# Performance work log

Hardware: AMD Instinct MI355X
Metric: run time of the kernel (lower is better)

Reference implementation:

```python
import jax, jax.numpy as jnp
import numpy as np

EMBED = 1024
NUM_EXPERTS = 8
ACTIVE = 2
HIDDEN = 4 * EMBED


def setup_inputs() -> dict:
    key = jax.random.key(0)
    ks = jax.random.split(key, 7)
    B, T = 4, 1024
    s1 = 1.0 / np.sqrt(EMBED)
    s2 = 1.0 / np.sqrt(HIDDEN)
    return {
        "x": jax.random.normal(ks[0], (B, T, EMBED), dtype=jnp.float32),
        # stacked expert weights, layout [in, out] (torch Linear applies x @ W.T + b)
        "W1": jax.random.uniform(ks[1], (NUM_EXPERTS, EMBED, HIDDEN), jnp.float32, -s1, s1),
        "b1": jax.random.uniform(ks[2], (NUM_EXPERTS, HIDDEN), jnp.float32, -s1, s1),
        "W2": jax.random.uniform(ks[3], (NUM_EXPERTS, HIDDEN, EMBED), jnp.float32, -s2, s2),
        "b2": jax.random.uniform(ks[4], (NUM_EXPERTS, EMBED), jnp.float32, -s2, s2),
        "Wr": jax.random.uniform(ks[5], (EMBED, NUM_EXPERTS), jnp.float32, -s1, s1),
        "br": jax.random.uniform(ks[6], (NUM_EXPERTS,), jnp.float32, -s1, s1),
    }


def reference(x, W1, b1, W2, b2, Wr, br):
    # ---- router (TopkRouter) ----
    scores = x @ Wr + br                                  # [B,T,E]
    topk_scores, indices = jax.lax.top_k(scores, ACTIVE)  # [B,T,K]
    # mask = zeros scattered with topk scores at topk positions (others stay 0),
    # then softmax over ALL experts (faithful to the reference's quirky softmax).
    one_hot = jax.nn.one_hot(indices, NUM_EXPERTS, dtype=scores.dtype)  # [B,T,K,E]
    mask = jnp.einsum('btke,btk->bte', one_hot, topk_scores)            # [B,T,E]
    router_output = jax.nn.softmax(mask, axis=-1)                       # [B,T,E]

    # ---- dense all-experts FFN (Expert): relu(x@W1+b1)@W2+b2 per expert ----
    h = jax.nn.relu(jnp.einsum('btd,edh->bteh', x, W1) + b1)            # [B,T,E,H]
    expert_outputs = jnp.einsum('bteh,ehd->bted', h, W2) + b2           # [B,T,E,D]

    # ---- weighted combine ----
    return jnp.einsum('bte,bted->btd', router_output, expert_outputs)   # [B,T,D]
```

## Files before the change

kernel.cpp:

```cpp
#include <hip/hip_runtime.h>
#include <hip/hip_bf16.h>
#include <cstdint>
#include <cstddef>

#define EMBED  1024
#define NEXP   8
#define HIDDEN 4096
#define TOKENS 4096

typedef __attribute__((ext_vector_type(8))) short bf16x8;
typedef __attribute__((ext_vector_type(4))) float f32x4;
using bf16 = __hip_bfloat16;

__device__ __forceinline__ void gload_lds16(const void* g, void* l) {
    __builtin_amdgcn_global_load_lds((const __attribute__((address_space(1))) void*)g,
                                     (__attribute__((address_space(3))) void*)l,
                                     16, 0, 0);
}

__device__ __forceinline__ int swz(int b) { return b ^ (((b >> 7) & 7) << 4); }

__global__ void cvt_kernel(const float* __restrict__ in, bf16* __restrict__ out, size_t n) {
    size_t i = ((size_t)blockIdx.x * blockDim.x + threadIdx.x) * 4;
    if (i + 3 < n) {
        float4 v = *(const float4*)(in + i);
        out[i + 0] = __float2bfloat16(v.x);
        out[i + 1] = __float2bfloat16(v.y);
        out[i + 2] = __float2bfloat16(v.z);
        out[i + 3] = __float2bfloat16(v.w);
    }
}

__global__ void transpose_cvt(const float* __restrict__ in, bf16* __restrict__ out,
                              int K, int N, size_t in_estride, size_t out_eoff, int ldo) {
    const int e = blockIdx.z;
    const float* ine = in + (size_t)e * in_estride;
    bf16* oute = out + (size_t)e * out_eoff;
    __shared__ float tile[32][33];
    const int n0 = blockIdx.x * 32, k0 = blockIdx.y * 32;
    const int tx = threadIdx.x, ty = threadIdx.y;
    #pragma unroll
    for (int i = ty; i < 32; i += 8)
        tile[i][tx] = ine[(size_t)(k0 + i) * N + n0 + tx];
    __syncthreads();
    #pragma unroll
    for (int i = ty; i < 32; i += 8)
        oute[(size_t)(n0 + i) * ldo + k0 + tx] = __float2bfloat16(tile[tx][i]);
}

__global__ void router_kernel(const float* __restrict__ x, const float* __restrict__ Wr,
                              const float* __restrict__ br, float* __restrict__ w) {
    const int t = blockIdx.x;
    const int lane = threadIdx.x;
    const float* xt = x + (size_t)t * EMBED;
    float s[NEXP];
    #pragma unroll
    for (int e = 0; e < NEXP; e++) s[e] = 0.f;
    for (int k = lane; k < EMBED; k += 64) {
        const float xv = xt[k];
        const float* wrk = Wr + (size_t)k * NEXP;
        #pragma unroll
        for (int e = 0; e < NEXP; e++) s[e] = fmaf(xv, wrk[e], s[e]);
    }
    #pragma unroll
    for (int e = 0; e < NEXP; e++) {
        #pragma unroll
        for (int off = 32; off >= 1; off >>= 1)
            s[e] += __shfl_xor(s[e], off);
    }
    if (lane == 0) {
        float sc[NEXP];
        #pragma unroll
        for (int e = 0; e < NEXP; e++) sc[e] = s[e] + br[e];
        int i1 = 0; float m1 = sc[0];
        #pragma unroll
        for (int e = 1; e < NEXP; e++) if (sc[e] > m1) { m1 = sc[e]; i1 = e; }
        int i2 = -1; float m2 = -1e30f;
        #pragma unroll
        for (int e = 0; e < NEXP; e++) if (e != i1 && sc[e] > m2) { m2 = sc[e]; i2 = e; }
        const float mx = fmaxf(m1, 0.f);
        const float denom = 6.f * expf(0.f - mx) + expf(m1 - mx) + expf(m2 - mx);
        #pragma unroll
        for (int e = 0; e < NEXP; e++) {
            float v = (e == i1) ? m1 : ((e == i2) ? m2 : 0.f);
            w[(size_t)t * NEXP + e] = expf(v - mx) / denom;
        }
    }
}


#define BARX()  { __builtin_amdgcn_sched_barrier(0); __builtin_amdgcn_s_barrier(); __builtin_amdgcn_sched_barrier(0); }
#define LGKM0() { asm volatile("s_waitcnt lgkmcnt(0)" ::: "memory"); __builtin_amdgcn_sched_barrier(0); }

#define PIPE_PREAMBLE(Abase, Bbase, lda, ldb)                                        \
    __shared__ __align__(16) bf16 As[2][2][128 * 64];                                \
    __shared__ __align__(16) bf16 Bs[2][2][128 * 64];                                \
    const int tid = threadIdx.x;                                                     \
    const int lane = tid & 63, wid = tid >> 6;                                       \
    const int mhalf = wid >> 2, wB = wid & 3;                                        \
    const int nhalf = wB >> 1, nsub = wB & 1;                                        \
    const int wv_r = mhalf * 128, wv_c = wB * 64;                                    \
    f32x4 acc[8][4] = {};                                                            \
    int rowloc[2], colel[2];                                                         \
    _Pragma("unroll")                                                                \
    for (int j = 0; j < 2; j++) {                                                    \
        int bs = swz(tid * 16 + j * 8192);                                           \
        rowloc[j] = bs >> 7; colel[j] = (bs & 127) >> 1;                             \
    }                                                                                \
    const bf16* pA0 = (Abase) + (size_t)(brow + rowloc[0]) * (lda) + colel[0];       \
    const bf16* pA1 = (Abase) + (size_t)(brow + rowloc[1]) * (lda) + colel[1];       \
    const bf16* pB0 = (Bbase) + (size_t)(bcol + rowloc[0]) * (ldb) + colel[0];       \
    const bf16* pB1 = (Bbase) + (size_t)(bcol + rowloc[1]) * (ldb) + colel[1];       \
    const int fr = lane & 15, kb0 = (lane >> 4) * 16;                                \
    const int xm = (fr & 7) << 4;                                                    \
    const int baA0 = (fr * 128 + kb0) ^ xm, baA1 = (fr * 128 + kb0 + 64) ^ xm;       \
    const int brB = (nsub * 64 + fr) * 128;                                          \
    const int baB0 = (brB + kb0) ^ xm, baB1 = (brB + kb0 + 64) ^ xm;

#define STAGE_A(bi, h, koff, lda)                                                    \
    do {                                                                             \
        gload_lds16(pA0 + (size_t)(h) * 128 * (lda) + (koff), &As[bi][h][tid * 8]);  \
        gload_lds16(pA1 + (size_t)(h) * 128 * (lda) + (koff), &As[bi][h][tid * 8 + 4096]); \
    } while (0)
#define STAGE_B(bi, h, koff, ldb)                                                    \
    do {                                                                             \
        gload_lds16(pB0 + (size_t)(h) * 128 * (ldb) + (koff), &Bs[bi][h][tid * 8]);  \
        gload_lds16(pB1 + (size_t)(h) * 128 * (ldb) + (koff), &Bs[bi][h][tid * 8 + 4096]); \
    } while (0)

#define MFMA_Q(mh, nh)                                                               \
    __builtin_amdgcn_s_setprio(1);                                                   \
    _Pragma("unroll")                                                                \
    for (int mm = 0; mm < 4; mm++)                                                   \
        _Pragma("unroll")                                                            \
        for (int nn = 0; nn < 2; nn++) {                                             \
            acc[(mh)*4+mm][(nh)*2+nn] = __builtin_amdgcn_mfma_f32_16x16x32_bf16(     \
                a[(mh)*4+mm][0], b[(nh)*2+nn][0], acc[(mh)*4+mm][(nh)*2+nn], 0,0,0); \
            acc[(mh)*4+mm][(nh)*2+nn] = __builtin_amdgcn_mfma_f32_16x16x32_bf16(     \
                a[(mh)*4+mm][1], b[(nh)*2+nn][1], acc[(mh)*4+mm][(nh)*2+nn], 0,0,0); \
        }                                                                            \
    __builtin_amdgcn_s_setprio(0);

#define PIPE_KLOOP(NT, lda, ldb)                                                     \
    STAGE_A(0, 0, 0, lda); STAGE_A(0, 1, 0, lda);                                    \
    STAGE_B(0, 0, 0, ldb); STAGE_B(0, 1, 0, ldb);                                    \
    STAGE_A(1, 0, 64, lda); STAGE_A(1, 1, 64, lda);                                  \
    STAGE_B(1, 0, 64, ldb); STAGE_B(1, 1, 64, ldb);                                  \
    asm volatile("s_waitcnt vmcnt(8)" ::: "memory");                                 \
    BARX();                                                                          \
    for (int t = 0; t < (NT); ++t) {                                                 \
        const int bi = t & 1;                                                        \
        const bool st = (t + 2) < (NT);                                              \
        const size_t koff = (size_t)(t + 2) * 64;                                    \
        const char* Ah = (const char*)&As[bi][mhalf][0];                             \
        const char* Bh = (const char*)&Bs[bi][nhalf][0];                             \
        bf16x8 a[8][2], b[4][2];                                                     \
                             \
        _Pragma("unroll")                                                            \
        for (int m = 0; m < 4; m++) {                                                \
            a[m][0] = *(const bf16x8*)(Ah + baA0 + m * 2048);                        \
            a[m][1] = *(const bf16x8*)(Ah + baA1 + m * 2048);                        \
        }                                                                            \
        _Pragma("unroll")                                                            \
        for (int n = 0; n < 2; n++) {                                                \
            b[n][0] = *(const bf16x8*)(Bh + baB0 + n * 2048);                        \
            b[n][1] = *(const bf16x8*)(Bh + baB1 + n * 2048);                        \
        }                                                                            \
        BARX(); LGKM0();                                                             \
        MFMA_Q(0, 0)                                                                 \
        BARX();                                                                      \
                             \
        _Pragma("unroll")                                                            \
        for (int m = 4; m < 8; m++) {                                                \
            a[m][0] = *(const bf16x8*)(Ah + baA0 + m * 2048);                        \
            a[m][1] = *(const bf16x8*)(Ah + baA1 + m * 2048);                        \
        }                                                                            \
        _Pragma("unroll")                                                            \
        for (int n = 2; n < 4; n++) {                                                \
            b[n][0] = *(const bf16x8*)(Bh + baB0 + n * 2048);                        \
            b[n][1] = *(const bf16x8*)(Bh + baB1 + n * 2048);                        \
        }                                                                            \
        BARX(); LGKM0();                                                             \
        MFMA_Q(0, 1)                                                                 \
        BARX();                                                                      \
                \
        if (st) { STAGE_A(bi, 0, koff, lda); STAGE_A(bi, 1, koff, lda); }            \
        MFMA_Q(1, 0)                                                                 \
        BARX();                                                                      \
                      \
        if (st) { STAGE_B(bi, 0, koff, ldb); STAGE_B(bi, 1, koff, ldb); }            \
        MFMA_Q(1, 1)                                                                 \
        if (st) { asm volatile("s_waitcnt vmcnt(8)" ::: "memory"); }                 \
        else    { asm volatile("s_waitcnt vmcnt(0)" ::: "memory"); }                 \
        BARX();                                                                      \
    }

__global__ __launch_bounds__(512, 2) void gemm1(const bf16* __restrict__ A,
                                                const bf16* __restrict__ Bt,
                                                const float* __restrict__ b1,
                                                const float* __restrict__ rw,
                                                bf16* __restrict__ H) {
    const int e = blockIdx.z;
    const int brow = blockIdx.y * 256;
    const int bcol = blockIdx.x * 256;
    const bf16* Be = Bt + (size_t)e * HIDDEN * EMBED;
    bf16* He = H + (size_t)e * TOKENS * HIDDEN;

    PIPE_PREAMBLE(A, Be, EMBED, EMBED)
    PIPE_KLOOP(16, EMBED, EMBED)

    #pragma unroll
    for (int n = 0; n < 4; n++) {
        const int col = bcol + wv_c + n * 16 + fr;
        const float bias = b1[e * HIDDEN + col];
        #pragma unroll
        for (int m = 0; m < 8; m++) {
            const int rowb = brow + wv_r + m * 16 + (lane >> 4) * 4;
            #pragma unroll
            for (int j = 0; j < 4; j++) {
                const int row = rowb + j;
                float v = acc[m][n][j] + bias;
                v = fmaxf(v, 0.f) * rw[(size_t)row * NEXP + e];
                He[(size_t)row * HIDDEN + col] = __float2bfloat16(v);
            }
        }
    }
}

__global__ __launch_bounds__(512, 2) void gemm2(const bf16* __restrict__ A,
                                                const bf16* __restrict__ Bt,
                                                const float* __restrict__ b2,
                                                const float* __restrict__ rw,
                                                float* __restrict__ out) {
    const int e = blockIdx.z;
    const int brow = blockIdx.y * 256;
    const int bcol = blockIdx.x * 256;
    const bf16* Ae = A + (size_t)e * TOKENS * HIDDEN;
    const bf16* Be = Bt + (size_t)e * EMBED * HIDDEN;

    PIPE_PREAMBLE(Ae, Be, HIDDEN, HIDDEN)
    PIPE_KLOOP(64, HIDDEN, HIDDEN)

    #pragma unroll
    for (int n = 0; n < 4; n++) {
        const int col = bcol + wv_c + n * 16 + fr;
        #pragma unroll
        for (int m = 0; m < 8; m++) {
            const int rowb = brow + wv_r + m * 16 + (lane >> 4) * 4;
            #pragma unroll
            for (int j = 0; j < 4; j++) {
                const int row = rowb + j;
                float v = acc[m][n][j];
                if (e == 0) {
                    const float* wrow = rw + (size_t)row * NEXP;
                    float s = 0.f;
                    #pragma unroll
                    for (int ee = 0; ee < NEXP; ee++) s = fmaf(wrow[ee], b2[ee * EMBED + col], s);
                    v += s;
                }
                atomicAdd(out + (size_t)row * EMBED + col, v);
            }
        }
    }
}

extern "C" void kernel_launch(void* const* d_in, const int* in_sizes, int n_in,
                              void* d_out, int out_size, void* d_ws, size_t ws_size,
                              hipStream_t stream) {
    const float* x  = (const float*)d_in[0];
    const float* W1 = (const float*)d_in[1];
    const float* b1 = (const float*)d_in[2];
    const float* W2 = (const float*)d_in[3];
    const float* b2 = (const float*)d_in[4];
    const float* Wr = (const float*)d_in[5];
    const float* br = (const float*)d_in[6];
    float* out = (float*)d_out;

    uint8_t* ws = (uint8_t*)d_ws;
    size_t off = 0;
    auto walloc = [&](size_t bytes) -> void* {
        void* p = ws + off;
        off += (bytes + 255) & ~(size_t)255;
        return p;
    };
    float* rw  = (float*)walloc((size_t)TOKENS * NEXP * 4);
    bf16* xb   = (bf16*)walloc((size_t)TOKENS * EMBED * 2);
    bf16* w1t  = (bf16*)walloc((size_t)NEXP * HIDDEN * EMBED * 2);
    bf16* w2t  = (bf16*)walloc((size_t)NEXP * EMBED * HIDDEN * 2);
    bf16* hbuf = (bf16*)walloc((size_t)NEXP * TOKENS * HIDDEN * 2);

    hipMemsetAsync(d_out, 0, (size_t)out_size * sizeof(float), stream);

    cvt_kernel<<<4096, 256, 0, stream>>>(x, xb, (size_t)TOKENS * EMBED);

    dim3 tb(32, 8);
    transpose_cvt<<<dim3(HIDDEN / 32, EMBED / 32, NEXP), tb, 0, stream>>>(
        W1, w1t, EMBED, HIDDEN, (size_t)EMBED * HIDDEN, (size_t)HIDDEN * EMBED, EMBED);
    transpose_cvt<<<dim3(EMBED / 32, HIDDEN / 32, NEXP), tb, 0, stream>>>(
        W2, w2t, HIDDEN, EMBED, (size_t)HIDDEN * EMBED, (size_t)EMBED * HIDDEN, HIDDEN);

    router_kernel<<<TOKENS, 64, 0, stream>>>(x, Wr, br, rw);

    gemm1<<<dim3(HIDDEN / 256, TOKENS / 256, NEXP), 512, 0, stream>>>(xb, w1t, b1, rw, hbuf);
    gemm2<<<dim3(EMBED / 256, TOKENS / 256, NEXP), 512, 0, stream>>>(hbuf, w2t, b2, rw, out);
}
```

Before: 950.6 us.

## Rewrite gemm1 with 128x128 triple-buffered tiles and remap gemm2 workgroup order

gemm1 moves from a 256x256 tile with 512 threads to a 128x128 tile with 256 threads. It uses a 3-stage LDS ring with a K step of 32, a new swizzle, and a 1D grid whose block indices are remapped across XCDs. gemm2's K-loop reorders its LDS fragment reads and its A/B staging so that loads overlap better with MFMA quarters, and it gains a similar XCD-aware 1D block index remap. The aims are higher occupancy and better L2 locality per chiplet. The risks are lower per-block data reuse in gemm1 and new scheduling hazards from the reordered barriers.

```diff
diff --git a/kernel.cpp b/kernel.cpp
--- a/kernel.cpp
+++ b/kernel.cpp
@@ -18,7 +18,8 @@
                                      16, 0, 0);
 }
 
-__device__ __forceinline__ int swz(int b) { return b ^ (((b >> 7) & 7) << 4); }
+__device__ __forceinline__ int swzA(int b) { return b ^ (((b >> 7) & 3) << 4); }
+__device__ __forceinline__ int swzB(int b) { return b ^ (((b >> 7) & 7) << 4); }
 
 __global__ void cvt_kernel(const float* __restrict__ in, bf16* __restrict__ out, size_t n) {
     size_t i = ((size_t)blockIdx.x * blockDim.x + threadIdx.x) * 4;
@@ -88,6 +89,109 @@
     }
 }
 
+
+#define G1_PREAMBLE(Abase, Bbase, lda, ldb)                                              \
+    __shared__ __align__(16) bf16 As[3][128 * 32];                                       \
+    __shared__ __align__(16) bf16 Bs[3][128 * 32];                                       \
+    const int tid = threadIdx.x;                                                         \
+    f32x4 acc[4][4] = {};                                                                \
+    int srow[2], scol[2];                                                                \
+    _Pragma("unroll")                                                                    \
+    for (int j = 0; j < 2; j++) {                                                        \
+        int b0 = tid * 16 + j * 4096;                                                    \
+        int bs = swzA(b0);                                                               \
+        srow[j] = bs >> 6; scol[j] = (bs & 63) >> 1;                                     \
+    }                                                                                    \
+    const bf16* ga0 = (Abase) + (size_t)(brow + srow[0]) * (lda) + scol[0];              \
+    const bf16* ga1 = (Abase) + (size_t)(brow + srow[1]) * (lda) + scol[1];              \
+    const bf16* gb0 = (Bbase) + (size_t)(bcol + srow[0]) * (ldb) + scol[0];              \
+    const bf16* gb1 = (Bbase) + (size_t)(bcol + srow[1]) * (ldb) + scol[1];              \
+    const int lane = tid & 63, wid = tid >> 6;                                           \
+    const int wv_r = (wid >> 1) * 64, wv_c = (wid & 1) * 64;                             \
+    const int fr = lane & 15, kbyte = (lane >> 4) * 16;                                  \
+    int offA[4], offB[4];                                                                \
+    _Pragma("unroll")                                                                    \
+    for (int m = 0; m < 4; m++) {                                                        \
+        offA[m] = swzA((wv_r + m * 16 + fr) * 64 + kbyte);                               \
+        offB[m] = swzA((wv_c + m * 16 + fr) * 64 + kbyte);                               \
+    }
+
+#define G1_STAGE(s, kt)                                                                  \
+    do {                                                                                 \
+        gload_lds16(ga0 + (kt), &As[s][tid * 8]);                                        \
+        gload_lds16(ga1 + (kt), &As[s][tid * 8 + 2048]);                                 \
+        gload_lds16(gb0 + (kt), &Bs[s][tid * 8]);                                        \
+        gload_lds16(gb1 + (kt), &Bs[s][tid * 8 + 2048]);                                 \
+    } while (0)
+
+#define G1_KLOOP(NT)                                                                     \
+    G1_STAGE(0, 0);                                                                      \
+    G1_STAGE(1, 32);                                                                     \
+    {                                                                                    \
+        int slot = 0, nslot = 2;                                                         \
+        for (int t = 0; t < (NT); ++t) {                                                 \
+            if (t + 2 < (NT)) { G1_STAGE(nslot, (t + 2) * 32); }                         \
+            if (t < (NT) - 2)       asm volatile("s_waitcnt vmcnt(8)" ::: "memory");     \
+            else if (t == (NT) - 2) asm volatile("s_waitcnt vmcnt(4)" ::: "memory");     \
+            else                    asm volatile("s_waitcnt vmcnt(0)" ::: "memory");     \
+            __builtin_amdgcn_s_barrier();                                                \
+            __builtin_amdgcn_sched_barrier(0);                                           \
+            const char* Ab = (const char*)As[slot];                                      \
+            const char* Bb = (const char*)Bs[slot];                                      \
+            bf16x8 af[4], bfr[4];                                                        \
+            _Pragma("unroll")                                                            \
+            for (int m = 0; m < 4; m++) af[m] = *(const bf16x8*)(Ab + offA[m]);          \
+            _Pragma("unroll")                                                            \
+            for (int n = 0; n < 4; n++) bfr[n] = *(const bf16x8*)(Bb + offB[n]);         \
+            __builtin_amdgcn_s_setprio(1);                                               \
+            _Pragma("unroll")                                                            \
+            for (int m = 0; m < 4; m++)                                                  \
+                _Pragma("unroll")                                                        \
+                for (int n = 0; n < 4; n++)                                              \
+                    acc[m][n] = __builtin_amdgcn_mfma_f32_16x16x32_bf16(af[m], bfr[n],   \
+                                                                       acc[m][n], 0, 0, 0); \
+            __builtin_amdgcn_s_setprio(0);                                               \
+            asm volatile("" ::: "memory");                                               \
+            __builtin_amdgcn_s_barrier();                                                \
+            slot = (slot == 2) ? 0 : slot + 1;                                           \
+            nslot = (nslot == 2) ? 0 : nslot + 1;                                        \
+        }                                                                                \
+    }
+
+__global__ __launch_bounds__(256, 3) void gemm1(const bf16* __restrict__ A,
+                                                const bf16* __restrict__ Bt,
+                                                const float* __restrict__ b1,
+                                                const float* __restrict__ rw,
+                                                bf16* __restrict__ H) {
+    const int wg = blockIdx.x;
+    const int sw = (wg & 7) * 1024 + (wg >> 3);
+    const int e  = sw >> 10;
+    const int rem = sw & 1023;
+    const int brow = (rem >> 5) * 128;
+    const int bcol = (rem & 31) * 128;
+    const bf16* Be = Bt + (size_t)e * HIDDEN * EMBED;
+    bf16* He = H + (size_t)e * TOKENS * HIDDEN;
+
+    G1_PREAMBLE(A, Be, EMBED, EMBED)
+    G1_KLOOP(EMBED / 32)
+
+    #pragma unroll
+    for (int n = 0; n < 4; n++) {
+        const int col = bcol + wv_c + n * 16 + fr;
+        const float bias = b1[e * HIDDEN + col];
+        #pragma unroll
+        for (int m = 0; m < 4; m++) {
+            const int rowb = brow + wv_r + m * 16 + (lane >> 4) * 4;
+            #pragma unroll
+            for (int j = 0; j < 4; j++) {
+                const int row = rowb + j;
+                float v = acc[m][n][j] + bias;
+                v = fmaxf(v, 0.f) * rw[(size_t)row * NEXP + e];
+                He[(size_t)row * HIDDEN + col] = __float2bfloat16(v);
+            }
+        }
+    }
+}
 
 #define BARX()  { __builtin_amdgcn_sched_barrier(0); __builtin_amdgcn_s_barrier(); __builtin_amdgcn_sched_barrier(0); }
 #define LGKM0() { asm volatile("s_waitcnt lgkmcnt(0)" ::: "memory"); __builtin_amdgcn_sched_barrier(0); }
@@ -104,7 +208,7 @@
     int rowloc[2], colel[2];                                                         \
     _Pragma("unroll")                                                                \
     for (int j = 0; j < 2; j++) {                                                    \
-        int bs = swz(tid * 16 + j * 8192);                                           \
+        int bs = swzB(tid * 16 + j * 8192);                                          \
         rowloc[j] = bs >> 7; colel[j] = (bs & 127) >> 1;                             \
     }                                                                                \
     const bf16* pA0 = (Abase) + (size_t)(brow + rowloc[0]) * (lda) + colel[0];       \
@@ -155,7 +259,7 @@
         const char* Ah = (const char*)&As[bi][mhalf][0];                             \
         const char* Bh = (const char*)&Bs[bi][nhalf][0];                             \
         bf16x8 a[8][2], b[4][2];                                                     \
-                             \
+                                        \
         _Pragma("unroll")                                                            \
         for (int m = 0; m < 4; m++) {                                                \
             a[m][0] = *(const bf16x8*)(Ah + baA0 + m * 2048);                        \
@@ -168,73 +272,44 @@
         }                                                                            \
         BARX(); LGKM0();                                                             \
         MFMA_Q(0, 0)                                                                 \
+             \
+        _Pragma("unroll")                                                            \
+        for (int n = 2; n < 4; n++) {                                                \
+            b[n][0] = *(const bf16x8*)(Bh + baB0 + n * 2048);                        \
+            b[n][1] = *(const bf16x8*)(Bh + baB1 + n * 2048);                        \
+        }                                                                            \
+        BARX(); LGKM0();                                                             \
+        MFMA_Q(0, 1)                                                                 \
         BARX();                                                                      \
-                             \
+           \
         _Pragma("unroll")                                                            \
         for (int m = 4; m < 8; m++) {                                                \
             a[m][0] = *(const bf16x8*)(Ah + baA0 + m * 2048);                        \
             a[m][1] = *(const bf16x8*)(Ah + baA1 + m * 2048);                        \
         }                                                                            \
-        _Pragma("unroll")                                                            \
-        for (int n = 2; n < 4; n++) {                                                \
-            b[n][0] = *(const bf16x8*)(Bh + baB0 + n * 2048);                        \
-            b[n][1] = *(const bf16x8*)(Bh + baB1 + n * 2048);                        \
-        }                                                                            \
+        if (st) { STAGE_B(bi, 0, koff, ldb); STAGE_B(bi, 1, koff, ldb); }            \
         BARX(); LGKM0();                                                             \
-        MFMA_Q(0, 1)                                                                 \
-        BARX();                                                                      \
-                \
-        if (st) { STAGE_A(bi, 0, koff, lda); STAGE_A(bi, 1, koff, lda); }            \
         MFMA_Q(1, 0)                                                                 \
         BARX();                                                                      \
-                      \
-        if (st) { STAGE_B(bi, 0, koff, ldb); STAGE_B(bi, 1, koff, ldb); }            \
+             \
+        if (st) { STAGE_A(bi, 0, koff, lda); STAGE_A(bi, 1, koff, lda); }            \
         MFMA_Q(1, 1)                                                                 \
         if (st) { asm volatile("s_waitcnt vmcnt(8)" ::: "memory"); }                 \
         else    { asm volatile("s_waitcnt vmcnt(0)" ::: "memory"); }                 \
         BARX();                                                                      \
     }
-
-__global__ __launch_bounds__(512, 2) void gemm1(const bf16* __restrict__ A,
-                                                const bf16* __restrict__ Bt,
-                                                const float* __restrict__ b1,
-                                                const float* __restrict__ rw,
-                                                bf16* __restrict__ H) {
-    const int e = blockIdx.z;
-    const int brow = blockIdx.y * 256;
-    const int bcol = blockIdx.x * 256;
-    const bf16* Be = Bt + (size_t)e * HIDDEN * EMBED;
-    bf16* He = H + (size_t)e * TOKENS * HIDDEN;
-
-    PIPE_PREAMBLE(A, Be, EMBED, EMBED)
-    PIPE_KLOOP(16, EMBED, EMBED)
-
-    #pragma unroll
-    for (int n = 0; n < 4; n++) {
-        const int col = bcol + wv_c + n * 16 + fr;
-        const float bias = b1[e * HIDDEN + col];
-        #pragma unroll
-        for (int m = 0; m < 8; m++) {
-            const int rowb = brow + wv_r + m * 16 + (lane >> 4) * 4;
-            #pragma unroll
-            for (int j = 0; j < 4; j++) {
-                const int row = rowb + j;
-                float v = acc[m][n][j] + bias;
-                v = fmaxf(v, 0.f) * rw[(size_t)row * NEXP + e];
-                He[(size_t)row * HIDDEN + col] = __float2bfloat16(v);
-            }
-        }
-    }
-}
 
 __global__ __launch_bounds__(512, 2) void gemm2(const bf16* __restrict__ A,
                                                 const bf16* __restrict__ Bt,
                                                 const float* __restrict__ b2,
                                                 const float* __restrict__ rw,
                                                 float* __restrict__ out) {
-    const int e = blockIdx.z;
-    const int brow = blockIdx.y * 256;
-    const int bcol = blockIdx.x * 256;
+    const int wg = blockIdx.x;
+    const int sw = (wg & 7) * 64 + (wg >> 3);
+    const int brow = (sw >> 5) * 256;
+    const int rem = sw & 31;
+    const int e = rem >> 2;
+    const int bcol = (rem & 3) * 256;
     const bf16* Ae = A + (size_t)e * TOKENS * HIDDEN;
     const bf16* Be = Bt + (size_t)e * EMBED * HIDDEN;
 
@@ -301,6 +376,6 @@
 
     router_kernel<<<TOKENS, 64, 0, stream>>>(x, Wr, br, rw);
 
-    gemm1<<<dim3(HIDDEN / 256, TOKENS / 256, NEXP), 512, 0, stream>>>(xb, w1t, b1, rw, hbuf);
-    gemm2<<<dim3(EMBED / 256, TOKENS / 256, NEXP), 512, 0, stream>>>(hbuf, w2t, b2, rw, out);
-}
+    gemm1<<<8192, 256, 0, stream>>>(xb, w1t, b1, rw, hbuf);
+    gemm2<<<512, 512, 0, stream>>>(hbuf, w2t, b2, rw, out);
+}
```

After: 898.7 us. 5.5% less time.
